# Kernel optimization log

Hardware: AMD Instinct MI355X
Metric: run time of the kernel (lower is better)

Reference implementation:

```python
import jax, jax.numpy as jnp
import numpy as np

K = 3
STRIDE = 1
PAD = 1
DIL = 1


def _unfold(a):
    # a: (N, C, H, W) -> patches (N, C, K*K, oH, oW), matching torch.F.unfold
    # channel-major ordering (c slowest, then kernel row, then kernel col).
    N, C, H, W = a.shape
    oH = (H + 2 * PAD - DIL * (K - 1) - 1) // STRIDE + 1
    oW = (W + 2 * PAD - DIL * (K - 1) - 1) // STRIDE + 1
    ap = jnp.pad(a, ((0, 0), (0, 0), (PAD, PAD), (PAD, PAD)))
    cols = []
    for i in range(K):
        for j in range(K):
            cols.append(ap[:, :,
                           i * DIL: i * DIL + (oH - 1) * STRIDE + 1: STRIDE,
                           j * DIL: j * DIL + (oW - 1) * STRIDE + 1: STRIDE])
    return jnp.stack(cols, axis=2)  # (N, C, K*K, oH, oW)


def setup_inputs() -> dict:
    key = jax.random.key(0)
    k1, k2, k3, k4, k5 = jax.random.split(key, 5)
    N, C, O, H, W = 4, 128, 256, 128, 128
    x = jax.random.normal(k1, (N, C, H, W), dtype=jnp.float32)
    depth = jax.random.uniform(k2, (N, 1, H, W), dtype=jnp.float32)
    camera_params = jax.random.normal(k3, (N, 4), dtype=jnp.float32)
    weight = jax.random.normal(k4, (O, C, K, K), dtype=jnp.float32) * 0.05
    bias = jax.random.normal(k5, (O,), dtype=jnp.float32) * 0.05
    return {"x": x, "depth": depth, "camera_params": camera_params,
            "weight": weight, "bias": bias}


def reference(x, depth, camera_params, weight, bias):
    # camera_params is accepted but unused, mirroring the torch module.
    O, C = weight.shape[0], weight.shape[1]
    xp = _unfold(x)        # (N, C, kk, oH, oW)
    dp = _unfold(depth)    # (N, 1, kk, oH, oW)
    w = weight.reshape(O, C, K * K)
    # depth-modulated im2col GEMM: sum_{c,p} w[o,c,p] * x_patch * d_patch
    out = jnp.einsum('ocp,ncpxy->noxy', w, xp * dp)
    return out + bias[None, :, None, None]
```

## Files before the change

### kernel.cpp

```cpp
#include <hip/hip_runtime.h>
#include <stdint.h>


#define C_IN 128
#define O_OUT 256
#define HW 128
#define NB 4
#define PADW 130

#define XD_ELEMS ((size_t)NB * PADW * PADW * C_IN)
#define XD_BYTES (XD_ELEMS * 2)
#define WT_ELEMS ((size_t)O_OUT * C_IN * 9)
#define WT_BYTES (WT_ELEMS * 2)

typedef __attribute__((ext_vector_type(8))) short short8;
typedef __attribute__((ext_vector_type(4))) float f32x4;
typedef __attribute__((ext_vector_type(2))) float f32x2;
typedef __attribute__((ext_vector_type(4))) unsigned uint4v;

__device__ __forceinline__ unsigned f2bf_bits(float f) {
  unsigned u = __builtin_bit_cast(unsigned, f);
  return (u + 0x7fffu + ((u >> 16) & 1u)) >> 16;
}

__device__ __forceinline__ void async_load16(const void* g, void* l) {
  __builtin_amdgcn_global_load_lds(
      (__attribute__((address_space(1))) void*)g,
      (__attribute__((address_space(3))) void*)l, 16, 0, 0);
}

__global__ __launch_bounds__(256) void prep_all(const float* __restrict__ x,
                                                const float* __restrict__ depth,
                                                const float* __restrict__ w,
                                                short* __restrict__ xd,
                                                short* __restrict__ wt) {
  const int R = blockIdx.x;

  if (R >= NB * HW + NB) {
    int gid = (R - (NB * HW + NB)) * 4608 + threadIdx.x;
#pragma unroll
    for (int i = 0; i < 18; ++i, gid += 256) {
      const int c = gid & 127;
      const int tap = (gid >> 7) % 9;
      const int o = gid / 1152;
      wt[gid] = (short)f2bf_bits(w[((size_t)o * C_IN + c) * 9 + tap]);
    }
    return;
  }

  if (R >= NB * HW) {
    const int n = R - NB * HW;
    uint4v* base0 = (uint4v*)(xd + (size_t)n * PADW * PADW * C_IN);
    uint4v* base1 = (uint4v*)(xd + ((size_t)n * PADW + (PADW - 1)) * PADW * C_IN);
    const uint4v z = {0u, 0u, 0u, 0u};
    const int per_row = PADW * C_IN * 2 / 16;
    for (int i = threadIdx.x; i < per_row; i += 256) {
      base0[i] = z;
      base1[i] = z;
    }
    return;
  }

  __shared__ short s[C_IN * PADW];

  const int n = R >> 7, y = R & 127;
  const int tid = threadIdx.x;
  const int lane = tid & 63;
  const int wave = tid >> 6;

  {
    unsigned* row = (unsigned*)(xd + ((size_t)(n * PADW + y + 1) * PADW) * C_IN);
    if (tid < 64) row[tid] = 0u;
    else if (tid < 128) row[(size_t)(PADW - 1) * 64 + (tid - 64)] = 0u;
  }

  const f32x2 d2 = *(const f32x2*)(depth + ((size_t)n * HW + y) * HW + 2 * lane);
  const float* xrow = x + (((size_t)n * C_IN) * HW + y) * HW + 2 * lane;
  unsigned* s32 = (unsigned*)s;
#pragma unroll 8
  for (int ci = 0; ci < 32; ++ci) {
    const int c = ci * 4 + wave;
    const f32x2 v = *(const f32x2*)(xrow + (size_t)c * HW * HW);
    s32[c * 65 + lane] = f2bf_bits(v.x * d2.x) | (f2bf_bits(v.y * d2.y) << 16);
  }
  __syncthreads();

  const unsigned short* s16 = (const unsigned short*)s;
  unsigned* orow = (unsigned*)(xd + ((size_t)(n * PADW + y + 1) * PADW + 1) * C_IN);
#pragma unroll 8
  for (int i = 0; i < 32; ++i) {
    const int flat = tid + i * 256;
    const int px = flat >> 6, cp = flat & 63;
    const unsigned lo = s16[(2 * cp) * PADW + px];
    const unsigned hi = s16[(2 * cp + 1) * PADW + px];
    orow[flat] = lo | (hi << 16);
  }
}

__global__ __launch_bounds__(256, 2) void conv_mfma(
    const short* __restrict__ xd, const short* __restrict__ wt,
    const float* __restrict__ bias, float* __restrict__ out) {
  __shared__ short lds[32768];

  const int tid = threadIdx.x;
  const int bx = blockIdx.x;
  const int n = bx >> 6;
  const int y = (bx & 63) << 1;
  const int o0 = blockIdx.y << 7;
  const int lane = tid & 63;
  const int wave = tid >> 6;
  const int wm = wave & 1, wn = wave >> 1;
  const int ln = lane & 15, q = lane >> 4;

  const int row0 = tid >> 2;
  const int part = tid & 3;

  const short* wg0 = wt + (size_t)(o0 + row0) * 1152 + part * 8;
  const short* wg1 = wg0 + (size_t)64 * 1152;
  const short* xh0 = xd + ((size_t)(n * PADW + y) * PADW + row0) * C_IN + part * 8;
  const short* xh1 = xh0 + (size_t)PADW * C_IN;

  f32x4 acc[4][8] = {};

  auto stageW = [&](int kt) {
    short* lb = lds + ((kt & 1) << 12) + tid * 8;
    const int wo = kt << 5;
    async_load16(wg0 + wo, lb);
    async_load16(wg1 + wo, lb + 2048);
  };
  auto stageX = [&](int kt) {
    const int tap = kt >> 2;
    const int cc = kt & 3;
    const int ti = tap / 3;
    const int tj = tap - ti * 3;
    const int xo = (ti * PADW + tj) * C_IN + (cc << 5);
    short* lb = lds + 8192 + (kt % 3) * 8192 + tid * 8;
    async_load16(xh0 + xo, lb);
    async_load16(xh0 + 64 * C_IN + xo, lb + 2048);
    async_load16(xh1 + xo, lb + 4096);
    async_load16(xh1 + 64 * C_IN + xo, lb + 6144);
  };

  stageW(0);
  stageX(0);
  stageX(1);

#pragma unroll 6
  for (int kt = 0; kt < 36; ++kt) {
    __syncthreads();

    if (kt + 1 < 36) stageW(kt + 1);
    if (kt + 2 < 36) stageX(kt + 2);

    const short* Ws = lds + ((kt & 1) << 12);
    const short* Xs = lds + 8192 + (kt % 3) * 8192;

    short8 a[4], b[8];
#pragma unroll
    for (int t = 0; t < 4; ++t)
      a[t] = *(const short8*)(Ws + (((wm << 6) + (t << 4) + ln) << 5) + (q << 3));
#pragma unroll
    for (int u = 0; u < 8; ++u)
      b[u] = *(const short8*)(Xs + (((wn << 7) + (u << 4) + ln) << 5) + (q << 3));
#pragma unroll
    for (int t = 0; t < 4; ++t)
#pragma unroll
      for (int u = 0; u < 8; ++u)
        acc[t][u] =
            __builtin_amdgcn_mfma_f32_16x16x32_bf16(a[t], b[u], acc[t][u], 0, 0, 0);
  }

#pragma unroll
  for (int t = 0; t < 4; ++t) {
    const int ob = o0 + (wm << 6) + (t << 4) + (q << 2);
#pragma unroll
    for (int u = 0; u < 8; ++u) {
      const int xcol = (u << 4) + ln;
      const int yrow = y + wn;
#pragma unroll
      for (int r = 0; r < 4; ++r) {
        const int o = ob + r;
        out[(((size_t)n * O_OUT + o) * HW + yrow) * HW + xcol] =
            acc[t][u][r] + bias[o];
      }
    }
  }
}

__global__ void conv_naive(const float* __restrict__ x,
                           const float* __restrict__ depth,
                           const float* __restrict__ w,
                           const float* __restrict__ bias,
                           float* __restrict__ out) {
  const int gid = blockIdx.x * 256 + threadIdx.x;
  if (gid >= NB * O_OUT * HW * HW) return;
  const int xc = gid & 127;
  const int y = (gid >> 7) & 127;
  const int o = (gid >> 14) & 255;
  const int n = gid >> 22;
  float s = bias[o];
  for (int c = 0; c < C_IN; ++c)
    for (int i = 0; i < 3; ++i) {
      const int yy = y + i - 1;
      if (yy < 0 || yy >= HW) continue;
      for (int j = 0; j < 3; ++j) {
        const int xx = xc + j - 1;
        if (xx < 0 || xx >= HW) continue;
        s += w[((o * C_IN + c) * 3 + i) * 3 + j] *
             x[(((size_t)n * C_IN + c) * HW + yy) * HW + xx] *
             depth[((size_t)n * HW + yy) * HW + xx];
      }
    }
  out[gid] = s;
}

extern "C" void kernel_launch(void* const* d_in, const int* in_sizes, int n_in,
                              void* d_out, int out_size, void* d_ws, size_t ws_size,
                              hipStream_t stream) {
  const float* x = (const float*)d_in[0];
  const float* depth = (const float*)d_in[1];
  const float* weight = (const float*)d_in[3];
  const float* bias = (const float*)d_in[4];
  float* out = (float*)d_out;

  const size_t need = XD_BYTES + WT_BYTES;
  if (ws_size < need) {
    conv_naive<<<(NB * O_OUT * HW * HW + 255) / 256, 256, 0, stream>>>(
        x, depth, weight, bias, out);
    return;
  }

  short* xd = (short*)d_ws;
  short* wt = (short*)((char*)d_ws + XD_BYTES);

  prep_all<<<NB * HW + NB + 64, 256, 0, stream>>>(x, depth, weight, xd, wt);
  conv_mfma<<<dim3(NB * HW / 2, 2), 256, 0, stream>>>(xd, wt, bias, out);
}
```

Measured before the change: 136.8 us.

## Load weights directly into registers in MFMA fragment order and reuse halo X tile

```diff
diff --git a/kernel.cpp b/kernel.cpp
--- a/kernel.cpp
+++ b/kernel.cpp
@@ -33,17 +33,26 @@
                                                 const float* __restrict__ depth,
                                                 const float* __restrict__ w,
                                                 short* __restrict__ xd,
-                                                short* __restrict__ wt) {
+                                                short* __restrict__ wt2) {
   const int R = blockIdx.x;
 
   if (R >= NB * HW + NB) {
     int gid = (R - (NB * HW + NB)) * 4608 + threadIdx.x;
 #pragma unroll
     for (int i = 0; i < 18; ++i, gid += 256) {
-      const int c = gid & 127;
-      const int tap = (gid >> 7) % 9;
-      const int o = gid / 1152;
-      wt[gid] = (short)f2bf_bits(w[((size_t)o * C_IN + c) * 9 + tap]);
+      const int j = gid & 7;
+      const int t = (gid >> 3) & 3;
+      const int lane = (gid >> 5) & 63;
+      const int wm = (gid >> 11) & 1;
+      const int g2 = gid >> 12;
+      const int s = g2 % 36;
+      const int o0 = g2 / 36;
+      const int ln = lane & 15, q = lane >> 4;
+      const int o = (o0 << 7) + (wm << 6) + (t << 4) + ln;
+      const int cc = s / 9;
+      const int tap = s % 9;
+      const int c = (cc << 5) + (q << 3) + j;
+      wt2[gid] = (short)f2bf_bits(w[((size_t)o * C_IN + c) * 9 + tap]);
     }
     return;
   }
@@ -98,81 +107,78 @@
 }
 
 __global__ __launch_bounds__(256, 2) void conv_mfma(
-    const short* __restrict__ xd, const short* __restrict__ wt,
+    const short* __restrict__ xd, const short* __restrict__ wt2,
     const float* __restrict__ bias, float* __restrict__ out) {
-  __shared__ short lds[32768];
+  __shared__ short xbuf[16640];
 
   const int tid = threadIdx.x;
   const int bx = blockIdx.x;
   const int n = bx >> 6;
   const int y = (bx & 63) << 1;
-  const int o0 = blockIdx.y << 7;
+  const int o0b = blockIdx.y;
   const int lane = tid & 63;
   const int wave = tid >> 6;
   const int wm = wave & 1, wn = wave >> 1;
   const int ln = lane & 15, q = lane >> 4;
 
-  const int row0 = tid >> 2;
-  const int part = tid & 3;
-
-  const short* wg0 = wt + (size_t)(o0 + row0) * 1152 + part * 8;
-  const short* wg1 = wg0 + (size_t)64 * 1152;
-  const short* xh0 = xd + ((size_t)(n * PADW + y) * PADW + row0) * C_IN + part * 8;
-  const short* xh1 = xh0 + (size_t)PADW * C_IN;
+  const short* wbase =
+      wt2 + (size_t)o0b * 147456 + (wm << 11) + (lane << 5);
+
+  const short* xsrc0 = xd + (size_t)(n * PADW + y) * PADW * C_IN +
+                       (tid >> 2) * C_IN + (tid & 3) * 8;
+  short* xdst0 = xbuf + tid * 8;
 
   f32x4 acc[4][8] = {};
-
-  auto stageW = [&](int kt) {
-    short* lb = lds + ((kt & 1) << 12) + tid * 8;
-    const int wo = kt << 5;
-    async_load16(wg0 + wo, lb);
-    async_load16(wg1 + wo, lb + 2048);
+  short8 areg[2][4];
+
+  auto loadA = [&](int s, int p) {
+#pragma unroll
+    for (int t = 0; t < 4; ++t)
+      areg[p][t] = *(const short8*)(wbase + (size_t)s * 4096 + t * 8);
   };
-  auto stageX = [&](int kt) {
-    const int tap = kt >> 2;
-    const int cc = kt & 3;
-    const int ti = tap / 3;
-    const int tj = tap - ti * 3;
-    const int xo = (ti * PADW + tj) * C_IN + (cc << 5);
-    short* lb = lds + 8192 + (kt % 3) * 8192 + tid * 8;
-    async_load16(xh0 + xo, lb);
-    async_load16(xh0 + 64 * C_IN + xo, lb + 2048);
-    async_load16(xh1 + xo, lb + 4096);
-    async_load16(xh1 + 64 * C_IN + xo, lb + 6144);
+  auto stageX = [&](int cc) {
+    const short* sp = xsrc0 + (cc << 5);
+#pragma unroll
+    for (int j = 0; j < 8; ++j)
+      async_load16(sp + j * 8192, xdst0 + j * 2048);
+    if (tid < 32) async_load16(sp + 8 * 8192, xdst0 + 8 * 2048);
   };
 
-  stageW(0);
+  loadA(0, 0);
   stageX(0);
-  stageX(1);
-
-#pragma unroll 6
-  for (int kt = 0; kt < 36; ++kt) {
-    __syncthreads();
-
-    if (kt + 1 < 36) stageW(kt + 1);
-    if (kt + 2 < 36) stageX(kt + 2);
-
-    const short* Ws = lds + ((kt & 1) << 12);
-    const short* Xs = lds + 8192 + (kt % 3) * 8192;
-
-    short8 a[4], b[8];
-#pragma unroll
-    for (int t = 0; t < 4; ++t)
-      a[t] = *(const short8*)(Ws + (((wm << 6) + (t << 4) + ln) << 5) + (q << 3));
-#pragma unroll
-    for (int u = 0; u < 8; ++u)
-      b[u] = *(const short8*)(Xs + (((wn << 7) + (u << 4) + ln) << 5) + (q << 3));
-#pragma unroll
-    for (int t = 0; t < 4; ++t)
+  __syncthreads();
+
+#pragma unroll
+  for (int cc = 0; cc < 4; ++cc) {
+#pragma unroll
+    for (int tap = 0; tap < 9; ++tap) {
+      const int s = cc * 9 + tap;
+      if (s + 1 < 36) loadA(s + 1, (s + 1) & 1);
+
+      const int ti = tap / 3, tj = tap % 3;
+      const int rbase = (wn + ti) * 130 + tj;
+
+      short8 b[8];
 #pragma unroll
       for (int u = 0; u < 8; ++u)
-        acc[t][u] =
-            __builtin_amdgcn_mfma_f32_16x16x32_bf16(a[t], b[u], acc[t][u], 0, 0, 0);
+        b[u] = *(const short8*)(xbuf + (rbase + (u << 4) + ln) * 32 + (q << 3));
+#pragma unroll
+      for (int t = 0; t < 4; ++t)
+#pragma unroll
+        for (int u = 0; u < 8; ++u)
+          acc[t][u] = __builtin_amdgcn_mfma_f32_16x16x32_bf16(
+              areg[s & 1][t], b[u], acc[t][u], 0, 0, 0);
+    }
+    if (cc + 1 < 4) {
+      __syncthreads();
+      stageX(cc + 1);
+      __syncthreads();
+    }
   }
 
 #pragma unroll
   for (int t = 0; t < 4; ++t) {
-    const int ob = o0 + (wm << 6) + (t << 4) + (q << 2);
+    const int ob = (o0b << 7) + (wm << 6) + (t << 4) + (q << 2);
 #pragma unroll
     for (int u = 0; u < 8; ++u) {
       const int xcol = (u << 4) + ln;
@@ -231,8 +237,8 @@
   }
 
   short* xd = (short*)d_ws;
-  short* wt = (short*)((char*)d_ws + XD_BYTES);
-
-  prep_all<<<NB * HW + NB + 64, 256, 0, stream>>>(x, depth, weight, xd, wt);
-  conv_mfma<<<dim3(NB * HW / 2, 2), 256, 0, stream>>>(xd, wt, bias, out);
-}
+  short* wt2 = (short*)((char*)d_ws + XD_BYTES);
+
+  prep_all<<<NB * HW + NB + 64, 256, 0, stream>>>(x, depth, weight, xd, wt2);
+  conv_mfma<<<dim3(NB * HW / 2, 2), 256, 0, stream>>>(xd, wt2, bias, out);
+}
```

Result: no change. 134.8 us (-1.4%).
